# Kernel tuning notes

Hardware: AMD Instinct MI355X
Metric: run time of the kernel (lower is better)

The kernel has to match this reference:

```python
import jax, jax.numpy as jnp
import numpy as np

N_NODES = 10000
N_EDGES = 320000
ND, ED = 256, 128
CAT = 2 * ND + ED  # 640


def setup_inputs() -> dict:
    key = jax.random.key(0)
    ks = jax.random.split(key, 12)
    s = 0.05
    inp = {
        'node_attr': jax.random.normal(ks[0], (N_NODES, ND), jnp.float32),
        'edge_attr': jax.random.normal(ks[1], (N_EDGES, ED), jnp.float32),
        'edge_index': jax.random.randint(ks[2], (2, N_EDGES), 0, N_NODES, jnp.int32),
        'mw0': jax.random.normal(ks[3], (CAT, ND), jnp.float32) * s,
        'mb0': jnp.zeros((ND,), jnp.float32),
        'mw1': jax.random.normal(ks[4], (ND, ND), jnp.float32) * s,
        'mb1': jnp.zeros((ND,), jnp.float32),
        'mw2': jax.random.normal(ks[5], (ND, ND), jnp.float32) * s,
        'mb2': jnp.zeros((ND,), jnp.float32),
        'ew0': jax.random.normal(ks[6], (CAT, ED), jnp.float32) * s,
        'eb0': jnp.zeros((ED,), jnp.float32),
        'ew1': jax.random.normal(ks[7], (ED, ED), jnp.float32) * s,
        'eb1': jnp.zeros((ED,), jnp.float32),
        'ew2': jax.random.normal(ks[8], (ED, ED), jnp.float32) * s,
        'eb2': jnp.zeros((ED,), jnp.float32),
        'aw': jax.random.normal(ks[9], (CAT, 1), jnp.float32) * s,
        'ab': jnp.zeros((1,), jnp.float32),
    }
    return inp


def _mlp3(f, w0, b0, w1, b1, w2, b2):
    h = jax.nn.relu(f @ w0 + b0)
    h = jax.nn.relu(h @ w1 + b1)
    return h @ w2 + b2


def reference(node_attr, edge_attr, edge_index,
              mw0, mb0, mw1, mb1, mw2, mb2,
              ew0, eb0, ew1, eb1, ew2, eb2, aw, ab):
    n = node_attr.shape[0]
    src, dst = edge_index[0], edge_index[1]
    # [E, 2*ND+ED] gathered per-edge features
    feat = jnp.concatenate([node_attr[src], node_attr[dst], edge_attr], axis=-1)

    messages = _mlp3(feat, mw0, mb0, mw1, mb1, mw2, mb2)        # [E, ND]
    att = (feat @ aw + ab)[:, 0]                                 # [E]

    # scatter_softmax over edges grouped by source node (stable)
    seg_max = jax.ops.segment_max(att, src, num_segments=n)
    seg_max = jnp.where(jnp.isfinite(seg_max), seg_max, 0.0)     # empty segments
    ex = jnp.exp(att - seg_max[src])
    denom = jax.ops.segment_sum(ex, src, num_segments=n)
    alpha = ex / denom[src]                                      # [E]

    x_out = jax.ops.segment_sum(alpha[:, None] * messages, src, num_segments=n)  # [N, ND]
    e_out = _mlp3(feat, ew0, eb0, ew1, eb1, ew2, eb2)            # [E, ED]
    return x_out, e_out
```

## Files before the change

kernel.cpp:

```cpp
#include <hip/hip_runtime.h>
#include <hip/hip_bf16.h>

#define N_NODES 10000
#define E_EDGES 320000
#define ND 256
#define ED 128

#define B_AM   0
#define B_BM   5120000
#define B_AE   10240000
#define B_BE   12800000
#define B_P1   15360000
#define B_P2   15400960
#define B_XA   15441920
#define B_DEN  25681920
#define B_CNT  25722880
#define B_ROW  25763840
#define B_CUR  25804800
#define B_EID  25845760
#define B_WT   27125760

#define M0T 0
#define M1T 65536
#define M2T 196608
#define E0T 327680
#define E1T 360448
#define E2T 393216
#define NPT0 425984
#define NPSEC 65536

#define R0 0
#define R1 16384
#define R2 32768
#define R3 49152
#define AL_S  65536
#define SRC_S 65792
#define DST_S 66048
#define EID_S 66304
#define LDS_TOT 66560

#define BM 64
#define NTILES (E_EDGES / BM)

typedef float  float4v __attribute__((ext_vector_type(4)));
typedef short  short8  __attribute__((ext_vector_type(8)));

__device__ __forceinline__ unsigned short f2bf(float f) {
    unsigned int b = __float_as_uint(f);
    return (unsigned short)((b + 0x7FFFu + ((b >> 16) & 1u)) >> 16);
}
__device__ __forceinline__ float bf2f(unsigned short u) {
    return __uint_as_float(((unsigned int)u) << 16);
}
__device__ __forceinline__ unsigned int pkbf(float a, float b) {
    __hip_bfloat162 h = __float22bfloat162_rn(float2{a, b});
    return *(unsigned int*)&h;
}

__device__ __forceinline__ void bar_ldsonly() {
    asm volatile("s_waitcnt lgkmcnt(0)" ::: "memory");
    __builtin_amdgcn_s_barrier();
}

__global__ void k_init(float* xa, float* den, int* cnt, int* cur) {
    int i = blockIdx.x * blockDim.x + threadIdx.x;
    int st = gridDim.x * blockDim.x;
    for (int j = i; j < N_NODES * ND; j += st) xa[j] = 0.f;
    for (int j = i; j < N_NODES; j += st) { den[j] = 0.f; cnt[j] = 0; cur[j] = 0; }
}

__global__ void k_deg(const int* ei, int* cnt) {
    int e = blockIdx.x * 256 + threadIdx.x;
    if (e < E_EDGES) atomicAdd(&cnt[ei[e]], 1);
}

__global__ __launch_bounds__(1024) void k_scan(const int* cnt, int* rowstart) {
    __shared__ int wsum[16];
    int t = threadIdx.x, lane = t & 63, w = t >> 6;
    int base = t * 10;
    int loc[10];
    int s = 0;
    #pragma unroll
    for (int i = 0; i < 10; i++) {
        int idx = base + i;
        int v = (idx < N_NODES) ? cnt[idx] : 0;
        loc[i] = s; s += v;
    }
    int run = s;
    #pragma unroll
    for (int d = 1; d < 64; d <<= 1) {
        int u = __shfl_up(run, d);
        if (lane >= d) run += u;
    }
    if (lane == 63) wsum[w] = run;
    __syncthreads();
    if (w == 0 && lane < 16) {
        int v = wsum[lane];
        int r = v;
        #pragma unroll
        for (int d = 1; d < 16; d <<= 1) {
            int u = __shfl_up(r, d);
            if (lane >= d) r += u;
        }
        wsum[lane] = r - v;
    }
    __syncthreads();
    int ex = wsum[w] + run - s;
    #pragma unroll
    for (int i = 0; i < 10; i++) {
        int idx = base + i;
        if (idx < N_NODES) rowstart[idx] = ex + loc[i];
    }
}

__global__ void k_fill(const int* ei, const int* rowstart, int* cur, int* eidcsr) {
    int e = blockIdx.x * 256 + threadIdx.x;
    if (e >= E_EDGES) return;
    int s = ei[e];
    int p = atomicAdd(&cur[s], 1);
    eidcsr[rowstart[s] + p] = e;
}

__global__ void k_wconv(const float* mw0, const float* mw1, const float* mw2,
                        const float* ew0, const float* ew1, const float* ew2, char* wtb) {
    const int tot = 409600;
    for (int idx = blockIdx.x * blockDim.x + threadIdx.x; idx < tot;
         idx += gridDim.x * blockDim.x) {
        if (idx < 212992) {
            int local, K, N, base; const float* src;
            if (idx < 32768)       { local = idx;          K = 128; N = 256; src = mw0 + 512*256; base = M0T; }
            else if (idx < 98304)  { local = idx - 32768;  K = 256; N = 256; src = mw1;           base = M1T; }
            else if (idx < 163840) { local = idx - 98304;  K = 256; N = 256; src = mw2;           base = M2T; }
            else if (idx < 180224) { local = idx - 163840; K = 128; N = 128; src = ew0 + 512*128; base = E0T; }
            else if (idx < 196608) { local = idx - 180224; K = 128; N = 128; src = ew1;           base = E1T; }
            else                   { local = idx - 196608; K = 128; N = 128; src = ew2;           base = E2T; }
            int W4 = N / 4;
            int CF = W4 >> 4;
            int NK = K / 32;
            int t = local;
            int j    = t & 7;   t >>= 3;
            int lane = t & 63;  t >>= 6;
            int cf   = t % CF;  t /= CF;
            int kk   = t % NK;  t /= NK;
            int wc   = t;
            int col = wc * W4 + cf * 16 + (lane & 15);
            int k   = kk * 32 + (lane >> 4) * 8 + j;
            ((unsigned short*)(wtb + base))[local] = f2bf(src[k * N + col]);
        } else {
            int q = idx - 212992;
            int sec = q >> 15;
            int local = q & 32767;
            int t = local;
            int j    = t & 7;   t >>= 3;
            int lane = t & 63;  t >>= 6;
            int cf   = t & 1;   t >>= 1;
            int kk   = t & 7;   t >>= 3;
            int wc   = t;
            int col = wc * 32 + cf * 16 + (lane & 15);
            int k   = kk * 32 + (lane >> 4) * 8 + j;
            const float* src; int N;
            if (sec == 0)      { src = mw0;         N = 256; }
            else if (sec == 1) { src = mw0;         N = 256; col += 128; }
            else if (sec == 2) { src = mw0 + 65536; N = 256; }
            else if (sec == 3) { src = mw0 + 65536; N = 256; col += 128; }
            else if (sec == 4) { src = ew0;         N = 128; }
            else               { src = ew0 + 32768; N = 128; }
            ((unsigned short*)(wtb + NPT0 + sec * NPSEC))[local] = f2bf(src[k * N + col]);
        }
    }
}

__device__ __forceinline__ int np_addr(int row, int keb) {
    return row * 512 + (keb ^ ((row & 7) << 4));
}

__global__ __launch_bounds__(512, 2) void k_npgemm(const float* na, const float* mb0,
                                                   const float* eb0, char* wsb) {
    __shared__ char sm[32768];
    const int tid = threadIdx.x;
    const int lane = tid & 63, wv = tid >> 6;
    const int wr = wv >> 2, wc = wv & 3;
    const int l15 = lane & 15, lg = lane >> 4;
    const int n0 = blockIdx.x * 64;
    const int sec = blockIdx.y;

    const char* wt = wsb + B_WT + NPT0 + (size_t)sec * NPSEC + (size_t)wc * 16384;
    short8 bbuf[2][4];
    #pragma unroll
    for (int i = 0; i < 4; i++)
        bbuf[0][i] = *(const short8*)(wt + ((size_t)i * 64 + lane) * 16);

    {
        int r = tid >> 3, cq = tid & 7;
        int node = n0 + r;
        int sxor = (r & 7) << 4;
        if (node < N_NODES) {
            const float4* src = (const float4*)(na + (size_t)node * ND + cq * 32);
            #pragma unroll
            for (int g = 0; g < 4; g++) {
                float4 va = src[g*2], vb = src[g*2+1];
                uint4 pk = make_uint4(pkbf(va.x,va.y), pkbf(va.z,va.w),
                                      pkbf(vb.x,vb.y), pkbf(vb.z,vb.w));
                *(uint4*)(sm + np_addr(r, (cq*32 + g*8)*2)) = pk;
            }
        } else {
            #pragma unroll
            for (int g = 0; g < 4; g++)
                *(uint4*)(sm + np_addr(r, (cq*32 + g*8)*2)) = make_uint4(0,0,0,0);
        }
    }
    bar_ldsonly();

    const float4v vz = {0.f, 0.f, 0.f, 0.f};
    float4v acc[2][2];
    #pragma unroll
    for (int i = 0; i < 2; i++) { acc[i][0] = vz; acc[i][1] = vz; }

    short8 areg[2][2];
    #pragma unroll
    for (int rf = 0; rf < 2; rf++)
        areg[0][rf] = *(const short8*)(sm + np_addr(wr*32 + rf*16 + l15, lg*16));

    #pragma unroll
    for (int h = 0; h < 4; h++) {
        if (h + 1 < 4) {
            #pragma unroll
            for (int i = 0; i < 4; i++)
                bbuf[(h+1)&1][i] = *(const short8*)(wt + ((size_t)((h+1)*4 + i) * 64 + lane) * 16);
        }
        #pragma unroll
        for (int ks = 0; ks < 2; ks++) {
            int kstep = h * 2 + ks;
            if (kstep + 1 < 8) {
                int keb = (kstep + 1) * 64 + lg * 16;
                #pragma unroll
                for (int rf = 0; rf < 2; rf++)
                    areg[(kstep+1)&1][rf] = *(const short8*)(sm + np_addr(wr*32 + rf*16 + l15, keb));
            }
            #pragma unroll
            for (int rf = 0; rf < 2; rf++)
                #pragma unroll
                for (int cf = 0; cf < 2; cf++)
                    acc[rf][cf] = __builtin_amdgcn_mfma_f32_16x16x32_bf16(areg[kstep&1][rf], bbuf[h&1][ks*2+cf], acc[rf][cf], 0, 0, 0);
        }
    }
    const float* bias = nullptr;
    unsigned short* outp; int ostride; int coladd = 0;
    if (sec == 0)      { outp = (unsigned short*)(wsb + B_AM); ostride = 256; bias = mb0; }
    else if (sec == 1) { outp = (unsigned short*)(wsb + B_AM); ostride = 256; bias = mb0 + 128; coladd = 128; }
    else if (sec == 2) { outp = (unsigned short*)(wsb + B_BM); ostride = 256; }
    else if (sec == 3) { outp = (unsigned short*)(wsb + B_BM); ostride = 256; coladd = 128; }
    else if (sec == 4) { outp = (unsigned short*)(wsb + B_AE); ostride = 128; bias = eb0; }
    else               { outp = (unsigned short*)(wsb + B_BE); ostride = 128; }
    #pragma unroll
    for (int rf = 0; rf < 2; rf++)
        #pragma unroll
        for (int cf = 0; cf < 2; cf++) {
            int colLoc = wc * 32 + cf * 16 + l15;
            float b = bias ? bias[colLoc] : 0.f;
            #pragma unroll
            for (int j = 0; j < 4; j++) {
                int node = n0 + wr*32 + rf*16 + lg*4 + j;
                if (node < N_NODES)
                    outp[(size_t)node * ostride + coladd + colLoc] = f2bf(acc[rf][cf][j] + b);
            }
        }
}

__global__ __launch_bounds__(256) void k_p1p2(const float* na, const float* aw,
                                              const float* ab, char* wsb) {
    int t = blockIdx.x * 256 + threadIdx.x;
    int node = t >> 4, kc = t & 15;
    if (node >= N_NODES) return;
    const float4* row = (const float4*)(na + (size_t)node * ND + kc * 16);
    const float4* w1p = (const float4*)(aw + kc * 16);
    const float4* w2p = (const float4*)(aw + 256 + kc * 16);
    float s1 = 0.f, s2 = 0.f;
    #pragma unroll
    for (int i = 0; i < 4; i++) {
        float4 v = row[i], w1 = w1p[i], w2 = w2p[i];
        s1 += v.x*w1.x + v.y*w1.y + v.z*w1.z + v.w*w1.w;
        s2 += v.x*w2.x + v.y*w2.y + v.z*w2.z + v.w*w2.w;
    }
    s1 += __shfl_xor(s1, 1); s1 += __shfl_xor(s1, 2);
    s1 += __shfl_xor(s1, 4); s1 += __shfl_xor(s1, 8);
    s2 += __shfl_xor(s2, 1); s2 += __shfl_xor(s2, 2);
    s2 += __shfl_xor(s2, 4); s2 += __shfl_xor(s2, 8);
    if (kc == 0) {
        ((float*)(wsb + B_P1))[node] = s1 + ab[0];
        ((float*)(wsb + B_P2))[node] = s2;
    }
}

struct DP {
    const float* ea; const int* ei; const int* csr;
    const unsigned short* Am; const unsigned short* Bm;
    const unsigned short* Ae; const unsigned short* Be;
    const float* p1; const float* p2; const float* aw;
    const float* mb1; const float* mb2; const float* eb1; const float* eb2;
    const char* wtb;
    float* xa; float* den; float* eout;
};

__device__ __forceinline__ int pan_addr(int blo, int bhi, int row, int col) {
    int base = (col & 128) ? bhi : blo;
    return base + row * 256 + ((((col & 127)) * 2) ^ ((row & 7) << 4));
}
__device__ __forceinline__ int dump_addr(int row, int col) {
    return row * 1024 + (((col * 4)) ^ ((row & 15) << 6));
}

template<int KTOT, int NOUT, int EPI, int NXT_N>
__device__ __forceinline__ void do_gemm(char* sm, const DP& p,
                                        int a_lo, int a_hi, const char* wt,
                                        int h_lo, int h_hi, const float* bias,
                                        const char* wt_next, short8 (&bbuf)[2][4],
                                        int wr, int wc, int lane) {
    constexpr int WCOL = NOUT / 4;
    constexpr int CF   = WCOL / 16;
    constexpr int NK   = KTOT / 32;
    constexpr int KH   = NK * CF / 4;
    constexpr int NKH  = NK / KH;
    const int l15 = lane & 15, lg = lane >> 4;
    const float4v vz = {0.f, 0.f, 0.f, 0.f};
    float4v acc[2][CF];
    #pragma unroll
    for (int i = 0; i < 2; i++)
        #pragma unroll
        for (int j = 0; j < CF; j++) acc[i][j] = vz;
    bar_ldsonly();
    short8 areg[2][2];
    #pragma unroll
    for (int rf = 0; rf < 2; rf++)
        areg[0][rf] = *(const short8*)(sm + pan_addr(a_lo, a_hi, wr*32 + rf*16 + l15, lg*8));
    #pragma unroll
    for (int h = 0; h < KH; h++) {
        if (h + 1 < KH) {
            #pragma unroll
            for (int i = 0; i < 4; i++)
                bbuf[(h+1)&1][i] = *(const short8*)(wt + ((size_t)((h+1)*4 + i) * 64 + lane) * 16);
        } else if constexpr (NXT_N > 0) {
            #pragma unroll
            for (int i = 0; i < NXT_N; i++)
                bbuf[(h+1)&1][i] = *(const short8*)(wt_next + ((size_t)i * 64 + lane) * 16);
        }
        #pragma unroll
        for (int ks = 0; ks < NKH; ks++) {
            int kstep = h * NKH + ks;
            if (kstep + 1 < NK) {
                int ke = (kstep + 1) * 32 + lg * 8;
                #pragma unroll
                for (int rf = 0; rf < 2; rf++)
                    areg[(kstep+1)&1][rf] = *(const short8*)(sm + pan_addr(a_lo, a_hi, wr*32 + rf*16 + l15, ke));
            }
            #pragma unroll
            for (int rf = 0; rf < 2; rf++)
                #pragma unroll
                for (int cf = 0; cf < CF; cf++)
                    acc[rf][cf] = __builtin_amdgcn_mfma_f32_16x16x32_bf16(areg[kstep&1][rf], bbuf[h&1][ks*CF+cf], acc[rf][cf], 0, 0, 0);
        }
    }
    if constexpr (EPI == 2) bar_ldsonly();
    const int*   srcid = (const int*)(sm + SRC_S);
    const int*   dstid = (const int*)(sm + DST_S);
    const int*   eid   = (const int*)(sm + EID_S);
    const float* exv   = (const float*)(sm + AL_S);
    #pragma unroll
    for (int rf = 0; rf < 2; rf++)
        #pragma unroll
        for (int cf = 0; cf < CF; cf++) {
            int col = wc * WCOL + cf * 16 + l15;
            int row0 = wr * 32 + rf * 16 + lg * 4;
            if constexpr (EPI == 0 || EPI == 1 || EPI == 3) {
                float vv[4];
                #pragma unroll
                for (int j = 0; j < 4; j++) {
                    int row = row0 + j;
                    float v = acc[rf][cf][j];
                    if constexpr (EPI == 0)
                        v += bf2f(p.Am[(size_t)srcid[row] * ND + col]) + bf2f(p.Bm[(size_t)dstid[row] * ND + col]);
                    else if constexpr (EPI == 1)
                        v += bias[col];
                    else
                        v += bf2f(p.Ae[(size_t)srcid[row] * ED + col]) + bf2f(p.Be[(size_t)dstid[row] * ED + col]);
                    vv[j] = fmaxf(v, 0.f);
                }
                unsigned w01 = pkbf(vv[0], vv[1]);
                unsigned w23 = pkbf(vv[2], vv[3]);
                *(unsigned short*)(sm + pan_addr(h_lo, h_hi, row0 + 0, col)) = (unsigned short)w01;
                *(unsigned short*)(sm + pan_addr(h_lo, h_hi, row0 + 1, col)) = (unsigned short)(w01 >> 16);
                *(unsigned short*)(sm + pan_addr(h_lo, h_hi, row0 + 2, col)) = (unsigned short)w23;
                *(unsigned short*)(sm + pan_addr(h_lo, h_hi, row0 + 3, col)) = (unsigned short)(w23 >> 16);
            } else {
                #pragma unroll
                for (int j = 0; j < 4; j++) {
                    int row = row0 + j;
                    float v = acc[rf][cf][j];
                    if constexpr (EPI == 2) {
                        v = (v + p.mb2[col]) * exv[row];
                        *(float*)(sm + dump_addr(row, col)) = v;
                    } else {
                        v += p.eb2[col];
                        p.eout[(size_t)eid[row] * ED + col] = v;
                    }
                }
            }
        }
}

__global__ __launch_bounds__(512, 4) void k_main(DP p) {
    extern __shared__ char sm[];
    const int tid = threadIdx.x;
    const int lane = tid & 63, wv = tid >> 6;
    const int wr = wv >> 2, wc = wv & 3;
    const int s0 = blockIdx.x * BM;

    const char* wtE0 = p.wtb + E0T + (size_t)wc * 8192;
    const char* wtE1 = p.wtb + E1T + (size_t)wc * 8192;
    const char* wtE2 = p.wtb + E2T + (size_t)wc * 8192;
    const char* wtM0 = p.wtb + M0T + (size_t)wc * 16384;
    const char* wtM1 = p.wtb + M1T + (size_t)wc * 32768;
    const char* wtM2 = p.wtb + M2T + (size_t)wc * 32768;

    short8 bbuf[2][4];
    #pragma unroll
    for (int i = 0; i < 4; i++)
        bbuf[0][i] = *(const short8*)(wtE0 + ((size_t)i * 64 + lane) * 16);

    if (tid < BM) {
        int eid = p.csr[s0 + tid];
        ((int*)(sm + EID_S))[tid] = eid;
        ((int*)(sm + SRC_S))[tid] = p.ei[eid];
        ((int*)(sm + DST_S))[tid] = p.ei[E_EDGES + eid];
    }
    {
        int r = tid >> 3, cq = tid & 7;
        int eid = p.csr[s0 + r];
        const float4* src = (const float4*)(p.ea + (size_t)eid * ED + cq * 16);
        const float4* wvp = (const float4*)(p.aw + 512 + cq * 16);
        int s = (r & 7) << 4;
        float4 v0 = src[0], v1 = src[1], v2 = src[2], v3 = src[3];
        float4 w0 = wvp[0], w1 = wvp[1], w2 = wvp[2], w3 = wvp[3];
        float sd = v0.x*w0.x + v0.y*w0.y + v0.z*w0.z + v0.w*w0.w
                 + v1.x*w1.x + v1.y*w1.y + v1.z*w1.z + v1.w*w1.w
                 + v2.x*w2.x + v2.y*w2.y + v2.z*w2.z + v2.w*w2.w
                 + v3.x*w3.x + v3.y*w3.y + v3.z*w3.z + v3.w*w3.w;
        int cb = cq * 32;
        *(uint4*)(sm + R0 + r*256 + (cb ^ s)) =
            make_uint4(pkbf(v0.x,v0.y), pkbf(v0.z,v0.w), pkbf(v1.x,v1.y), pkbf(v1.z,v1.w));
        *(uint4*)(sm + R0 + r*256 + ((cb + 16) ^ s)) =
            make_uint4(pkbf(v2.x,v2.y), pkbf(v2.z,v2.w), pkbf(v3.x,v3.y), pkbf(v3.z,v3.w));
        sd += __shfl_xor(sd, 1); sd += __shfl_xor(sd, 2); sd += __shfl_xor(sd, 4);
        if (cq == 0) {
            int sn = p.ei[eid];
            int dn = p.ei[E_EDGES + eid];
            float a = sd + p.p1[sn] + p.p2[dn];
            float ex = __expf(a);
            ((float*)(sm + AL_S))[r] = ex;
            unsafeAtomicAdd(&p.den[sn], ex);
        }
    }
    do_gemm<128,128,3,4>(sm, p, R0, 0,  wtE0, R1, 0,  nullptr, wtE1, bbuf, wr, wc, lane);
    do_gemm<128,128,1,4>(sm, p, R1, 0,  wtE1, R2, 0,  p.eb1,   wtE2, bbuf, wr, wc, lane);
    do_gemm<128,128,4,4>(sm, p, R2, 0,  wtE2, 0,  0,  nullptr, wtM0, bbuf, wr, wc, lane);
    do_gemm<128,256,0,4>(sm, p, R0, 0,  wtM0, R1, R2, nullptr, wtM1, bbuf, wr, wc, lane);
    do_gemm<256,256,1,4>(sm, p, R1, R2, wtM1, R0, R3, p.mb1,   wtM2, bbuf, wr, wc, lane);
    do_gemm<256,256,2,0>(sm, p, R0, R3, wtM2, 0,  0,  nullptr, nullptr, bbuf, wr, wc, lane);
    bar_ldsonly();
    {
        const int* srcid = (const int*)(sm + SRC_S);
        int h = tid >> 8;
        int c = tid & 255;
        int rend = h * 32 + 31;
        float acc = 0.f;
        for (int r = h * 32; r <= rend; r++) {
            acc += *(const float*)(sm + dump_addr(r, c));
            if (r == rend || srcid[r + 1] != srcid[r]) {
                unsafeAtomicAdd(&p.xa[(size_t)srcid[r] * ND + c], acc);
                acc = 0.f;
            }
        }
    }
}

__global__ void k_norm(const float* xa, const float* den, float* xout) {
    int i = blockIdx.x * 256 + threadIdx.x;
    if (i >= N_NODES * ND) return;
    float d = den[i >> 8];
    xout[i] = (d > 0.f) ? xa[i] / d : 0.f;
}

extern "C" void kernel_launch(void* const* d_in, const int* in_sizes, int n_in,
                              void* d_out, int out_size, void* d_ws, size_t ws_size,
                              hipStream_t stream) {
    const float* na  = (const float*)d_in[0];
    const float* ea  = (const float*)d_in[1];
    const int*   ei  = (const int*)d_in[2];
    const float* mw0 = (const float*)d_in[3];
    const float* mb0 = (const float*)d_in[4];
    const float* mw1 = (const float*)d_in[5];
    const float* mb1 = (const float*)d_in[6];
    const float* mw2 = (const float*)d_in[7];
    const float* mb2 = (const float*)d_in[8];
    const float* ew0 = (const float*)d_in[9];
    const float* eb0 = (const float*)d_in[10];
    const float* ew1 = (const float*)d_in[11];
    const float* eb1 = (const float*)d_in[12];
    const float* ew2 = (const float*)d_in[13];
    const float* eb2 = (const float*)d_in[14];
    const float* aw  = (const float*)d_in[15];
    const float* ab  = (const float*)d_in[16];
    float* out = (float*)d_out;
    char*  wsb = (char*)d_ws;

    float* xout = out;
    float* eout = out + (size_t)N_NODES * ND;

    float* xa  = (float*)(wsb + B_XA);
    float* den = (float*)(wsb + B_DEN);
    int*   cnt = (int*)(wsb + B_CNT);
    int*   row = (int*)(wsb + B_ROW);
    int*   cur = (int*)(wsb + B_CUR);
    int*   eidcsr = (int*)(wsb + B_EID);

    k_init<<<512, 256, 0, stream>>>(xa, den, cnt, cur);
    k_deg<<<1250, 256, 0, stream>>>(ei, cnt);
    k_scan<<<1, 1024, 0, stream>>>(cnt, row);
    k_fill<<<1250, 256, 0, stream>>>(ei, row, cur, eidcsr);
    k_wconv<<<400, 256, 0, stream>>>(mw0, mw1, mw2, ew0, ew1, ew2, wsb + B_WT);
    k_npgemm<<<dim3(157, 6), 512, 0, stream>>>(na, mb0, eb0, wsb);
    k_p1p2<<<625, 256, 0, stream>>>(na, aw, ab, wsb);

    DP p{ea, ei, eidcsr,
         (const unsigned short*)(wsb + B_AM), (const unsigned short*)(wsb + B_BM),
         (const unsigned short*)(wsb + B_AE), (const unsigned short*)(wsb + B_BE),
         (const float*)(wsb + B_P1), (const float*)(wsb + B_P2), aw,
         mb1, mb2, eb1, eb2, (const char*)(wsb + B_WT), xa, den, eout};
    hipFuncSetAttribute((const void*)k_main, hipFuncAttributeMaxDynamicSharedMemorySize, LDS_TOT);
    k_main<<<NTILES, 512, LDS_TOT, stream>>>(p);
    k_norm<<<10000, 256, 0, stream>>>(xa, den, xout);
}
```

Measured before the change: 443.8 us.

## Split message MLP layers into column halves to cut LDS and raise occupancy

The second and third message-MLP layers are now split along the hidden dimension into two halves. Each half is computed as a 128-wide slice of layer 1 followed by a partial layer-2 product, with the layer-2 outputs accumulated directly into the node aggregate via segmented atomic adds in the GEMM epilogue. This drops the fourth LDS panel and the LDS dump/reduce pass, shrinking shared memory from about 66KB to about 50KB, and launch bounds rise from 4 to 6 blocks per CU. In exchange, the number of global atomics into xa roughly doubles, with flushes at most every 4 rows instead of every 32, and the extra GEMM phases add barriers.

After: 784.4 us. 76.7% more time.

```diff
diff --git a/kernel.cpp b/kernel.cpp
--- a/kernel.cpp
+++ b/kernel.cpp
@@ -20,24 +20,25 @@
 #define B_EID  25845760
 #define B_WT   27125760
 
-#define M0T 0
-#define M1T 65536
-#define M2T 196608
-#define E0T 327680
-#define E1T 360448
-#define E2T 393216
+#define M0T  0
+#define M1A  65536
+#define M1B  131072
+#define M2A  196608
+#define M2B  262144
+#define E0T  327680
+#define E1T  360448
+#define E2T  393216
 #define NPT0 425984
 #define NPSEC 65536
 
 #define R0 0
 #define R1 16384
 #define R2 32768
-#define R3 49152
-#define AL_S  65536
-#define SRC_S 65792
-#define DST_S 66048
-#define EID_S 66304
-#define LDS_TOT 66560
+#define AL_S  49152
+#define SRC_S 49408
+#define DST_S 49664
+#define EID_S 49920
+#define LDS_TOT 50176
 
 #define BM 64
 #define NTILES (E_EDGES / BM)
@@ -127,25 +128,24 @@
     for (int idx = blockIdx.x * blockDim.x + threadIdx.x; idx < tot;
          idx += gridDim.x * blockDim.x) {
         if (idx < 212992) {
-            int local, K, N, base; const float* src;
-            if (idx < 32768)       { local = idx;          K = 128; N = 256; src = mw0 + 512*256; base = M0T; }
-            else if (idx < 98304)  { local = idx - 32768;  K = 256; N = 256; src = mw1;           base = M1T; }
-            else if (idx < 163840) { local = idx - 98304;  K = 256; N = 256; src = mw2;           base = M2T; }
-            else if (idx < 180224) { local = idx - 163840; K = 128; N = 128; src = ew0 + 512*128; base = E0T; }
-            else if (idx < 196608) { local = idx - 180224; K = 128; N = 128; src = ew1;           base = E1T; }
-            else                   { local = idx - 196608; K = 128; N = 128; src = ew2;           base = E2T; }
-            int W4 = N / 4;
-            int CF = W4 >> 4;
-            int NK = K / 32;
+            int local; const float* src; int stride, colbase, W4, CF, NK, base;
+            if (idx < 32768)       { local=idx;        src=mw0+512*256; stride=256; colbase=0;   W4=64; CF=4; NK=4; base=M0T; }
+            else if (idx < 65536)  { local=idx-32768;  src=mw1;         stride=256; colbase=0;   W4=32; CF=2; NK=8; base=M1A; }
+            else if (idx < 98304)  { local=idx-65536;  src=mw1;         stride=256; colbase=128; W4=32; CF=2; NK=8; base=M1B; }
+            else if (idx < 131072) { local=idx-98304;  src=mw2;         stride=256; colbase=0;   W4=64; CF=4; NK=4; base=M2A; }
+            else if (idx < 163840) { local=idx-131072; src=mw2+128*256; stride=256; colbase=0;   W4=64; CF=4; NK=4; base=M2B; }
+            else if (idx < 180224) { local=idx-163840; src=ew0+512*128; stride=128; colbase=0;   W4=32; CF=2; NK=4; base=E0T; }
+            else if (idx < 196608) { local=idx-180224; src=ew1;         stride=128; colbase=0;   W4=32; CF=2; NK=4; base=E1T; }
+            else                   { local=idx-196608; src=ew2;         stride=128; colbase=0;   W4=32; CF=2; NK=4; base=E2T; }
             int t = local;
             int j    = t & 7;   t >>= 3;
             int lane = t & 63;  t >>= 6;
             int cf   = t % CF;  t /= CF;
             int kk   = t % NK;  t /= NK;
             int wc   = t;
-            int col = wc * W4 + cf * 16 + (lane & 15);
+            int col = colbase + wc * W4 + cf * 16 + (lane & 15);
             int k   = kk * 32 + (lane >> 4) * 8 + j;
-            ((unsigned short*)(wtb + base))[local] = f2bf(src[k * N + col]);
+            ((unsigned short*)(wtb + base))[local] = f2bf(src[k * stride + col]);
         } else {
             int q = idx - 212992;
             int sec = q >> 15;
@@ -193,7 +193,6 @@
     {
         int r = tid >> 3, cq = tid & 7;
         int node = n0 + r;
-        int sxor = (r & 7) << 4;
         if (node < N_NODES) {
             const float4* src = (const float4*)(na + (size_t)node * ND + cq * 32);
             #pragma unroll
@@ -305,9 +304,6 @@
 __device__ __forceinline__ int pan_addr(int blo, int bhi, int row, int col) {
     int base = (col & 128) ? bhi : blo;
     return base + row * 256 + ((((col & 127)) * 2) ^ ((row & 7) << 4));
-}
-__device__ __forceinline__ int dump_addr(int row, int col) {
-    return row * 1024 + (((col * 4)) ^ ((row & 15) << 6));
 }
 
 template<int KTOT, int NOUT, int EPI, int NXT_N>
@@ -360,7 +356,6 @@
                     acc[rf][cf] = __builtin_amdgcn_mfma_f32_16x16x32_bf16(areg[kstep&1][rf], bbuf[h&1][ks*CF+cf], acc[rf][cf], 0, 0, 0);
         }
     }
-    if constexpr (EPI == 2) bar_ldsonly();
     const int*   srcid = (const int*)(sm + SRC_S);
     const int*   dstid = (const int*)(sm + DST_S);
     const int*   eid   = (const int*)(sm + EID_S);
@@ -391,36 +386,46 @@
                 *(unsigned short*)(sm + pan_addr(h_lo, h_hi, row0 + 1, col)) = (unsigned short)(w01 >> 16);
                 *(unsigned short*)(sm + pan_addr(h_lo, h_hi, row0 + 2, col)) = (unsigned short)w23;
                 *(unsigned short*)(sm + pan_addr(h_lo, h_hi, row0 + 3, col)) = (unsigned short)(w23 >> 16);
-            } else {
+            } else if constexpr (EPI == 6 || EPI == 7) {
+                float run = 0.f;
                 #pragma unroll
                 for (int j = 0; j < 4; j++) {
                     int row = row0 + j;
                     float v = acc[rf][cf][j];
-                    if constexpr (EPI == 2) {
-                        v = (v + p.mb2[col]) * exv[row];
-                        *(float*)(sm + dump_addr(row, col)) = v;
-                    } else {
-                        v += p.eb2[col];
-                        p.eout[(size_t)eid[row] * ED + col] = v;
+                    if constexpr (EPI == 7) v += bias[col];
+                    run += v * exv[row];
+                    bool flush = (j == 3) || (srcid[row + 1] != srcid[row]);
+                    if (flush) {
+                        unsafeAtomicAdd(&p.xa[(size_t)srcid[row] * ND + col], run);
+                        run = 0.f;
                     }
                 }
+            } else {
+                #pragma unroll
+                for (int j = 0; j < 4; j++) {
+                    int row = row0 + j;
+                    float v = acc[rf][cf][j] + p.eb2[col];
+                    p.eout[(size_t)eid[row] * ED + col] = v;
+                }
             }
         }
 }
 
-__global__ __launch_bounds__(512, 4) void k_main(DP p) {
+__global__ __launch_bounds__(512, 6) void k_main(DP p) {
     extern __shared__ char sm[];
     const int tid = threadIdx.x;
     const int lane = tid & 63, wv = tid >> 6;
     const int wr = wv >> 2, wc = wv & 3;
     const int s0 = blockIdx.x * BM;
 
-    const char* wtE0 = p.wtb + E0T + (size_t)wc * 8192;
-    const char* wtE1 = p.wtb + E1T + (size_t)wc * 8192;
-    const char* wtE2 = p.wtb + E2T + (size_t)wc * 8192;
-    const char* wtM0 = p.wtb + M0T + (size_t)wc * 16384;
-    const char* wtM1 = p.wtb + M1T + (size_t)wc * 32768;
-    const char* wtM2 = p.wtb + M2T + (size_t)wc * 32768;
+    const char* wtE0  = p.wtb + E0T + (size_t)wc * 8192;
+    const char* wtE1  = p.wtb + E1T + (size_t)wc * 8192;
+    const char* wtE2  = p.wtb + E2T + (size_t)wc * 8192;
+    const char* wtM0  = p.wtb + M0T + (size_t)wc * 16384;
+    const char* wtM1a = p.wtb + M1A + (size_t)wc * 16384;
+    const char* wtM1b = p.wtb + M1B + (size_t)wc * 16384;
+    const char* wtM2a = p.wtb + M2A + (size_t)wc * 16384;
+    const char* wtM2b = p.wtb + M2B + (size_t)wc * 16384;
 
     short8 bbuf[2][4];
     #pragma unroll
@@ -460,27 +465,14 @@
             unsafeAtomicAdd(&p.den[sn], ex);
         }
     }
-    do_gemm<128,128,3,4>(sm, p, R0, 0,  wtE0, R1, 0,  nullptr, wtE1, bbuf, wr, wc, lane);
-    do_gemm<128,128,1,4>(sm, p, R1, 0,  wtE1, R2, 0,  p.eb1,   wtE2, bbuf, wr, wc, lane);
-    do_gemm<128,128,4,4>(sm, p, R2, 0,  wtE2, 0,  0,  nullptr, wtM0, bbuf, wr, wc, lane);
-    do_gemm<128,256,0,4>(sm, p, R0, 0,  wtM0, R1, R2, nullptr, wtM1, bbuf, wr, wc, lane);
-    do_gemm<256,256,1,4>(sm, p, R1, R2, wtM1, R0, R3, p.mb1,   wtM2, bbuf, wr, wc, lane);
-    do_gemm<256,256,2,0>(sm, p, R0, R3, wtM2, 0,  0,  nullptr, nullptr, bbuf, wr, wc, lane);
-    bar_ldsonly();
-    {
-        const int* srcid = (const int*)(sm + SRC_S);
-        int h = tid >> 8;
-        int c = tid & 255;
-        int rend = h * 32 + 31;
-        float acc = 0.f;
-        for (int r = h * 32; r <= rend; r++) {
-            acc += *(const float*)(sm + dump_addr(r, c));
-            if (r == rend || srcid[r + 1] != srcid[r]) {
-                unsafeAtomicAdd(&p.xa[(size_t)srcid[r] * ND + c], acc);
-                acc = 0.f;
-            }
-        }
-    }
+    do_gemm<128,128,3,4>(sm, p, R0, 0,  wtE0,  R1, 0,  nullptr,     wtE1,  bbuf, wr, wc, lane);
+    do_gemm<128,128,1,4>(sm, p, R1, 0,  wtE1,  R2, 0,  p.eb1,       wtE2,  bbuf, wr, wc, lane);
+    do_gemm<128,128,4,4>(sm, p, R2, 0,  wtE2,  0,  0,  nullptr,     wtM0,  bbuf, wr, wc, lane);
+    do_gemm<128,256,0,4>(sm, p, R0, 0,  wtM0,  R1, R2, nullptr,     wtM1a, bbuf, wr, wc, lane);
+    do_gemm<256,128,1,4>(sm, p, R1, R2, wtM1a, R0, 0,  p.mb1,       wtM2a, bbuf, wr, wc, lane);
+    do_gemm<128,256,6,4>(sm, p, R0, 0,  wtM2a, 0,  0,  nullptr,     wtM1b, bbuf, wr, wc, lane);
+    do_gemm<256,128,1,4>(sm, p, R1, R2, wtM1b, R0, 0,  p.mb1 + 128, wtM2b, bbuf, wr, wc, lane);
+    do_gemm<128,256,7,0>(sm, p, R0, 0,  wtM2b, 0,  0,  p.mb2,       nullptr, bbuf, wr, wc, lane);
 }
 
 __global__ void k_norm(const float* xa, const float* den, float* xout) {
```

## Shrink LDS footprint by splitting K=256 GEMMs and storing messages as bf16

Applied to the files above, without the earlier changes.

The 256-wide GEMMs are split into two K=128 halves that share an accumulator passed across calls, so each half reads a single 16KB panel. This frees one LDS region. The final weighted messages are stored as bf16 into the panel regions instead of an fp32 dump buffer, which lowers LDS use from about 65KB to about 49KB. With that, launch bounds are raised from 4 to 6 blocks per SM, and the A-fragment register double-buffering is removed. The risks are bf16 rounding of the messages before the segment reduction, register pressure at the higher occupancy target, and less latency hiding on the LDS reads.

New measurement: 653.5 us. +47.2%, slower.

```diff
diff --git a/kernel.cpp b/kernel.cpp
--- a/kernel.cpp
+++ b/kernel.cpp
@@ -32,12 +32,11 @@
 #define R0 0
 #define R1 16384
 #define R2 32768
-#define R3 49152
-#define AL_S  65536
-#define SRC_S 65792
-#define DST_S 66048
-#define EID_S 66304
-#define LDS_TOT 66560
+#define AL_S  49152
+#define SRC_S 49408
+#define DST_S 49664
+#define EID_S 49920
+#define LDS_TOT 50176
 
 #define BM 64
 #define NTILES (E_EDGES / BM)
@@ -193,7 +192,6 @@
     {
         int r = tid >> 3, cq = tid & 7;
         int node = n0 + r;
-        int sxor = (r & 7) << 4;
         if (node < N_NODES) {
             const float4* src = (const float4*)(na + (size_t)node * ND + cq * 32);
             #pragma unroll
@@ -306,33 +304,28 @@
     int base = (col & 128) ? bhi : blo;
     return base + row * 256 + ((((col & 127)) * 2) ^ ((row & 7) << 4));
 }
-__device__ __forceinline__ int dump_addr(int row, int col) {
-    return row * 1024 + (((col * 4)) ^ ((row & 15) << 6));
-}
-
-template<int KTOT, int NOUT, int EPI, int NXT_N>
+
+template<int NOUT, int EPI, int NXT_N, bool ZERO>
 __device__ __forceinline__ void do_gemm(char* sm, const DP& p,
                                         int a_lo, int a_hi, const char* wt,
                                         int h_lo, int h_hi, const float* bias,
                                         const char* wt_next, short8 (&bbuf)[2][4],
+                                        float4v (&acc)[2][4],
                                         int wr, int wc, int lane) {
     constexpr int WCOL = NOUT / 4;
     constexpr int CF   = WCOL / 16;
-    constexpr int NK   = KTOT / 32;
+    constexpr int NK   = 4;
     constexpr int KH   = NK * CF / 4;
     constexpr int NKH  = NK / KH;
     const int l15 = lane & 15, lg = lane >> 4;
-    const float4v vz = {0.f, 0.f, 0.f, 0.f};
-    float4v acc[2][CF];
-    #pragma unroll
-    for (int i = 0; i < 2; i++)
+    if constexpr (ZERO) {
+        const float4v vz = {0.f, 0.f, 0.f, 0.f};
         #pragma unroll
-        for (int j = 0; j < CF; j++) acc[i][j] = vz;
+        for (int i = 0; i < 2; i++)
+            #pragma unroll
+            for (int j = 0; j < CF; j++) acc[i][j] = vz;
+    }
     bar_ldsonly();
-    short8 areg[2][2];
-    #pragma unroll
-    for (int rf = 0; rf < 2; rf++)
-        areg[0][rf] = *(const short8*)(sm + pan_addr(a_lo, a_hi, wr*32 + rf*16 + l15, lg*8));
     #pragma unroll
     for (int h = 0; h < KH; h++) {
         if (h + 1 < KH) {
@@ -347,20 +340,19 @@
         #pragma unroll
         for (int ks = 0; ks < NKH; ks++) {
             int kstep = h * NKH + ks;
-            if (kstep + 1 < NK) {
-                int ke = (kstep + 1) * 32 + lg * 8;
-                #pragma unroll
-                for (int rf = 0; rf < 2; rf++)
-                    areg[(kstep+1)&1][rf] = *(const short8*)(sm + pan_addr(a_lo, a_hi, wr*32 + rf*16 + l15, ke));
-            }
+            int ke = kstep * 32 + lg * 8;
+            short8 a[2];
+            #pragma unroll
+            for (int rf = 0; rf < 2; rf++)
+                a[rf] = *(const short8*)(sm + pan_addr(a_lo, a_hi, wr*32 + rf*16 + l15, ke));
             #pragma unroll
             for (int rf = 0; rf < 2; rf++)
                 #pragma unroll
                 for (int cf = 0; cf < CF; cf++)
-                    acc[rf][cf] = __builtin_amdgcn_mfma_f32_16x16x32_bf16(areg[kstep&1][rf], bbuf[h&1][ks*CF+cf], acc[rf][cf], 0, 0, 0);
-        }
-    }
-    if constexpr (EPI == 2) bar_ldsonly();
+                    acc[rf][cf] = __builtin_amdgcn_mfma_f32_16x16x32_bf16(a[rf], bbuf[h&1][ks*CF+cf], acc[rf][cf], 0, 0, 0);
+        }
+    }
+    if constexpr (EPI == 5) return;
     const int*   srcid = (const int*)(sm + SRC_S);
     const int*   dstid = (const int*)(sm + DST_S);
     const int*   eid   = (const int*)(sm + EID_S);
@@ -391,24 +383,29 @@
                 *(unsigned short*)(sm + pan_addr(h_lo, h_hi, row0 + 1, col)) = (unsigned short)(w01 >> 16);
                 *(unsigned short*)(sm + pan_addr(h_lo, h_hi, row0 + 2, col)) = (unsigned short)w23;
                 *(unsigned short*)(sm + pan_addr(h_lo, h_hi, row0 + 3, col)) = (unsigned short)(w23 >> 16);
+            } else if constexpr (EPI == 8) {
+                float vv[4];
+                #pragma unroll
+                for (int j = 0; j < 4; j++)
+                    vv[j] = (acc[rf][cf][j] + bias[col]) * exv[row0 + j];
+                unsigned w01 = pkbf(vv[0], vv[1]);
+                unsigned w23 = pkbf(vv[2], vv[3]);
+                *(unsigned short*)(sm + pan_addr(h_lo, h_hi, row0 + 0, col)) = (unsigned short)w01;
+                *(unsigned short*)(sm + pan_addr(h_lo, h_hi, row0 + 1, col)) = (unsigned short)(w01 >> 16);
+                *(unsigned short*)(sm + pan_addr(h_lo, h_hi, row0 + 2, col)) = (unsigned short)w23;
+                *(unsigned short*)(sm + pan_addr(h_lo, h_hi, row0 + 3, col)) = (unsigned short)(w23 >> 16);
             } else {
                 #pragma unroll
                 for (int j = 0; j < 4; j++) {
                     int row = row0 + j;
-                    float v = acc[rf][cf][j];
-                    if constexpr (EPI == 2) {
-                        v = (v + p.mb2[col]) * exv[row];
-                        *(float*)(sm + dump_addr(row, col)) = v;
-                    } else {
-                        v += p.eb2[col];
-                        p.eout[(size_t)eid[row] * ED + col] = v;
-                    }
+                    float v = acc[rf][cf][j] + p.eb2[col];
+                    p.eout[(size_t)eid[row] * ED + col] = v;
                 }
             }
         }
 }
 
-__global__ __launch_bounds__(512, 4) void k_main(DP p) {
+__global__ __launch_bounds__(512, 6) void k_main(DP p) {
     extern __shared__ char sm[];
     const int tid = threadIdx.x;
     const int lane = tid & 63, wv = tid >> 6;
@@ -423,6 +420,7 @@
     const char* wtM2 = p.wtb + M2T + (size_t)wc * 32768;
 
     short8 bbuf[2][4];
+    float4v acc[2][4];
     #pragma unroll
     for (int i = 0; i < 4; i++)
         bbuf[0][i] = *(const short8*)(wtE0 + ((size_t)i * 64 + lane) * 16);
@@ -460,24 +458,26 @@
             unsafeAtomicAdd(&p.den[sn], ex);
         }
     }
-    do_gemm<128,128,3,4>(sm, p, R0, 0,  wtE0, R1, 0,  nullptr, wtE1, bbuf, wr, wc, lane);
-    do_gemm<128,128,1,4>(sm, p, R1, 0,  wtE1, R2, 0,  p.eb1,   wtE2, bbuf, wr, wc, lane);
-    do_gemm<128,128,4,4>(sm, p, R2, 0,  wtE2, 0,  0,  nullptr, wtM0, bbuf, wr, wc, lane);
-    do_gemm<128,256,0,4>(sm, p, R0, 0,  wtM0, R1, R2, nullptr, wtM1, bbuf, wr, wc, lane);
-    do_gemm<256,256,1,4>(sm, p, R1, R2, wtM1, R0, R3, p.mb1,   wtM2, bbuf, wr, wc, lane);
-    do_gemm<256,256,2,0>(sm, p, R0, R3, wtM2, 0,  0,  nullptr, nullptr, bbuf, wr, wc, lane);
+    do_gemm<128,3,4,true >(sm, p, R0, 0, wtE0,          R1, 0,  nullptr, wtE1,          bbuf, acc, wr, wc, lane);
+    do_gemm<128,1,4,true >(sm, p, R1, 0, wtE1,          R2, 0,  p.eb1,   wtE2,          bbuf, acc, wr, wc, lane);
+    do_gemm<128,4,4,true >(sm, p, R2, 0, wtE2,          0,  0,  nullptr, wtM0,          bbuf, acc, wr, wc, lane);
+    do_gemm<256,0,4,true >(sm, p, R0, 0, wtM0,          R1, R2, nullptr, wtM1,          bbuf, acc, wr, wc, lane);
+    do_gemm<256,5,4,true >(sm, p, R1, 0, wtM1,          0,  0,  nullptr, wtM1 + 16384,  bbuf, acc, wr, wc, lane);
+    do_gemm<256,1,4,false>(sm, p, R2, 0, wtM1 + 16384,  R0, R1, p.mb1,   wtM2,          bbuf, acc, wr, wc, lane);
+    do_gemm<256,5,4,true >(sm, p, R0, 0, wtM2,          0,  0,  nullptr, wtM2 + 16384,  bbuf, acc, wr, wc, lane);
+    do_gemm<256,8,0,false>(sm, p, R1, 0, wtM2 + 16384,  R0, R2, p.mb2,   nullptr,       bbuf, acc, wr, wc, lane);
     bar_ldsonly();
     {
         const int* srcid = (const int*)(sm + SRC_S);
         int h = tid >> 8;
         int c = tid & 255;
         int rend = h * 32 + 31;
-        float acc = 0.f;
+        float accr = 0.f;
         for (int r = h * 32; r <= rend; r++) {
-            acc += *(const float*)(sm + dump_addr(r, c));
+            accr += bf2f(*(const unsigned short*)(sm + pan_addr(R0, R2, r, c)));
             if (r == rend || srcid[r + 1] != srcid[r]) {
-                unsafeAtomicAdd(&p.xa[(size_t)srcid[r] * ND + c], acc);
-                acc = 0.f;
+                unsafeAtomicAdd(&p.xa[(size_t)srcid[r] * ND + c], accr);
+                accr = 0.f;
             }
         }
     }
```
